# Kernel tuning notes

Hardware: AMD Instinct MI355X
Metric: run time of the kernel (lower is better)

## Reference

```python
import jax, jax.numpy as jnp
import numpy as np

K = 20          # neighbors
T = 3           # time steps
GW = 10.0       # surrogate-gradient width
EPS = 1e-5      # batchnorm eps


def _knn_idx(f, k):
    # f: (B, N, C). torch code maximizes -||xi-xj||^2 via topk.
    x2 = jnp.sum(f * f, axis=-1)                          # (B, N)
    inner = jnp.einsum('bnc,bmc->bnm', f, f)              # (B, N, N)
    neg_d = 2.0 * inner - x2[:, :, None] - x2[:, None, :]
    return jax.lax.top_k(neg_d, k)[1]                     # (B, N, k)


def _graph_feature(f, k):
    # f: (B, N, C) -> (B, N, k, 2C) = cat(neighbor - center, neighbor)
    idx = _knn_idx(f, k)
    nb = jax.vmap(lambda ft, ix: ft[ix])(f, idx)          # (B, N, k, C)
    return jnp.concatenate([nb - f[:, :, None, :], nb], axis=-1)


def _bn(x, g, b, axes):
    # training-mode batchnorm (batch statistics), channel-last
    m = jnp.mean(x, axis=axes, keepdims=True)
    v = jnp.var(x, axis=axes, keepdims=True)
    return (x - m) * jax.lax.rsqrt(v + EPS) * g + b


def _lrelu(x):
    return jnp.where(x >= 0, x, 0.2 * x)


def _spike(x):
    # surrogate value + straight-through hard spike (training-mode detach trick)
    xc = jnp.clip(x, -10.0, 10.0)
    soft = 0.5 * jnp.exp(-0.5 * xc * xc) / np.sqrt(2.0 * np.pi) + 0.5 * jax.nn.sigmoid(GW * xc)
    hard = (x > 0).astype(x.dtype)
    return soft + jax.lax.stop_gradient(hard - soft)


def _lif(x, mem, thr, ref, md, ta, rd, tb):
    md = jnp.clip(md, 0.1, 0.99)
    ta = jnp.clip(ta, 0.001, 0.1)
    rd = jnp.clip(rd, 0.1, 0.95)
    x = x * (ref <= 0).astype(x.dtype)
    mem = mem * md * (1.0 - ref) + x
    s = _spike(mem - thr)
    mem = mem * (1.0 - s)
    ref = ref * rd + s
    thr = tb + (thr + ta * s - tb) * 0.95
    return s, mem, thr, ref


def _forward(x, W0, g0, b0, W1, g1, b1, W2, g2, b2, W3, g3, b3, Wm, gm, bm,
             l0md, l0ta, l0rd, l0tb, l1md, l1ta, l1rd, l1tb,
             l2md, l2ta, l2rd, l2tb, l3md, l3ta, l3rd, l3tb,
             lfmd, lfta, lfrd, lftb, tw):
    f0 = jnp.transpose(x, (0, 2, 1))                      # (B, N, 3)
    convs = [(W0, g0, b0), (W1, g1, b1), (W2, g2, b2), (W3, g3, b3)]
    lifs = [(l0md, l0ta, l0rd, l0tb), (l1md, l1ta, l1rd, l1tb),
            (l2md, l2ta, l2rd, l2tb), (l3md, l3ta, l3rd, l3tb)]
    states = [None] * 4
    pooled = []
    for t in range(T):
        cur = f0
        feats = []
        for i in range(4):
            gf = _graph_feature(cur, K)                   # (B, N, k, 2C)
            h = jnp.einsum('bnkc,oc->bnko', gf, convs[i][0])  # 1x1 conv
            h = _lrelu(_bn(h, convs[i][1], convs[i][2], (0, 1, 2)))
            h = jnp.max(h, axis=2)                        # max over k -> (B, N, O)
            md, ta, rd, tb = lifs[i]
            if states[i] is None:
                mem = jnp.zeros_like(h)
                thr = jnp.broadcast_to(tb, h.shape).astype(h.dtype)
                ref = jnp.zeros_like(h)
            else:
                # state manager detaches persisted states between calls
                mem, thr, ref = (jax.lax.stop_gradient(s) for s in states[i])
            s, mem, thr, ref = _lif(h, mem, thr, ref, md, ta, rd, tb)
            states[i] = (mem, thr, ref)
            feats.append(s)
            cur = s
        cat = jnp.concatenate(feats, axis=-1)             # (B, N, 960)
        agg = _lrelu(_bn(jnp.einsum('bnc,oc->bno', cat, Wm), gm, bm, (0, 1)))
        pooled.append(jnp.max(agg, axis=1))               # global max pool -> (B, 512)
    tf = jnp.stack(pooled, axis=0)                        # (T, B, 512)
    out = jnp.einsum('t,tbf->bf', jax.nn.softmax(tw), tf)
    mem = jnp.zeros_like(out)
    thr = jnp.broadcast_to(lftb, out.shape).astype(out.dtype)
    ref = jnp.zeros_like(out)
    s, _, _, _ = _lif(out, mem, thr, ref, lfmd, lfta, lfrd, lftb)
    return s


def setup_inputs() -> dict:
    key = jax.random.key(0)
    ks = iter(jax.random.split(key, 64))
    B, N = 2, 1024
    d = {}
    d['x'] = jax.random.normal(next(ks), (B, 3, N), jnp.float32)
    dims = [(64, 6), (128, 128), (256, 256), (512, 512)]  # (out, in) for 1x1 convs
    for i, (o, c) in enumerate(dims):
        d[f'W{i}'] = jax.random.normal(next(ks), (o, c), jnp.float32) / np.sqrt(c)
        d[f'g{i}'] = 1.0 + 0.1 * jax.random.normal(next(ks), (o,), jnp.float32)
        d[f'b{i}'] = 0.1 * jax.random.normal(next(ks), (o,), jnp.float32)
    d['Wm'] = jax.random.normal(next(ks), (512, 960), jnp.float32) / np.sqrt(960.0)
    d['gm'] = 1.0 + 0.1 * jax.random.normal(next(ks), (512,), jnp.float32)
    d['bm'] = 0.1 * jax.random.normal(next(ks), (512,), jnp.float32)
    for name, c in [('l0', 64), ('l1', 128), ('l2', 256), ('l3', 512), ('lf', 512)]:
        d[name + 'md'] = jnp.full((c,), 0.9, jnp.float32) + 0.02 * jax.random.normal(next(ks), (c,), jnp.float32)
        d[name + 'ta'] = jnp.full((c,), 0.01, jnp.float32) + 0.002 * jax.random.normal(next(ks), (c,), jnp.float32)
        d[name + 'rd'] = jnp.full((c,), 0.5, jnp.float32) + 0.02 * jax.random.normal(next(ks), (c,), jnp.float32)
        d[name + 'tb'] = jnp.ones((c,), jnp.float32) + 0.05 * jax.random.normal(next(ks), (c,), jnp.float32)
    d['tw'] = 1.0 + 0.1 * jax.random.normal(next(ks), (T,), jnp.float32)
    return d


def reference(x, W0, g0, b0, W1, g1, b1, W2, g2, b2, W3, g3, b3, Wm, gm, bm,
              l0md, l0ta, l0rd, l0tb, l1md, l1ta, l1rd, l1tb,
              l2md, l2ta, l2rd, l2tb, l3md, l3ta, l3rd, l3tb,
              lfmd, lfta, lfrd, lftb, tw):
    return _forward(x, W0, g0, b0, W1, g1, b1, W2, g2, b2, W3, g3, b3, Wm, gm, bm,
                    l0md, l0ta, l0rd, l0tb, l1md, l1ta, l1rd, l1tb,
                    l2md, l2ta, l2rd, l2tb, l3md, l3ta, l3rd, l3tb,
                    lfmd, lfta, lfrd, lftb, tw)
```

## Files before the change

kernel.cpp:

```cpp
#include <hip/hip_runtime.h>
#include <math.h>

#define NPTS 1024
#define BB 2
#define KNN 20
#define ROWS 2048
#define CATC 960
#define TT 3
#define IDXS 32
typedef unsigned long long ull;
typedef __attribute__((ext_vector_type(8))) short bf16x8;
typedef __attribute__((ext_vector_type(4))) float f32x4;

__device__ __forceinline__ float lrelu_f(float x){ return x >= 0.f ? x : 0.2f*x; }
__device__ __forceinline__ unsigned short f2bf(float f){
  unsigned u = __float_as_uint(f);
  return (unsigned short)((u + 0x7FFFu + ((u >> 16) & 1u)) >> 16);
}
__device__ __forceinline__ float bf2f(unsigned short h){ return __uint_as_float(((unsigned)h) << 16); }

__device__ __forceinline__ void stg_u32(unsigned* p, unsigned v){ __hip_atomic_store(p, v, __ATOMIC_RELAXED, __HIP_MEMORY_SCOPE_AGENT); }
__device__ __forceinline__ void stg_f64(double* p, double v){ __hip_atomic_store(p, v, __ATOMIC_RELAXED, __HIP_MEMORY_SCOPE_AGENT); }
__device__ __forceinline__ unsigned ldg_u32(const unsigned* p){ return __hip_atomic_load(p, __ATOMIC_RELAXED, __HIP_MEMORY_SCOPE_AGENT); }
__device__ __forceinline__ double ldg_f64(const double* p){ return __hip_atomic_load(p, __ATOMIC_RELAXED, __HIP_MEMORY_SCOPE_AGENT); }

__device__ __forceinline__ void mfma_dev(const short* __restrict__ A, int lda,
    const short* __restrict__ B3, size_t sStride, int ldb,
    float* __restrict__ C, int ldc, int K, int bm, int bn, int tid)
{
  const int wave = tid >> 6, lane = tid & 63;
  const int wm = (wave >> 1) << 5, wn = (wave & 1) << 5;
  const int rr = lane & 15, kq = (lane >> 4) << 3;
  f32x4 acc[2][2] = {};
  const short* Ap = A + (size_t)(bm + wm + rr)*lda + kq;
  const short* Bp = B3 + (size_t)(bn + wn + rr)*ldb + kq;
  for (int k0 = 0; k0 < K; k0 += 32) {
    bf16x8 a0 = *(const bf16x8*)(Ap + k0);
    bf16x8 a1 = *(const bf16x8*)(Ap + (size_t)16*lda + k0);
#pragma unroll
    for (int s = 0; s < 3; ++s) {
      bf16x8 b0 = *(const bf16x8*)(Bp + (size_t)s*sStride + k0);
      bf16x8 b1 = *(const bf16x8*)(Bp + (size_t)s*sStride + (size_t)16*ldb + k0);
      acc[0][0] = __builtin_amdgcn_mfma_f32_16x16x32_bf16(a0, b0, acc[0][0], 0, 0, 0);
      acc[0][1] = __builtin_amdgcn_mfma_f32_16x16x32_bf16(a0, b1, acc[0][1], 0, 0, 0);
      acc[1][0] = __builtin_amdgcn_mfma_f32_16x16x32_bf16(a1, b0, acc[1][0], 0, 0, 0);
      acc[1][1] = __builtin_amdgcn_mfma_f32_16x16x32_bf16(a1, b1, acc[1][1], 0, 0, 0);
    }
  }
  const int drb = (lane >> 4) << 2;
#pragma unroll
  for (int i = 0; i < 2; ++i)
#pragma unroll
    for (int j = 0; j < 2; ++j)
#pragma unroll
      for (int t = 0; t < 4; ++t)
        C[(size_t)(bm + wm + i*16 + drb + t)*ldc + bn + wn + j*16 + rr] = acc[i][j][t];
}

__device__ __forceinline__ void agg_tile(const short* __restrict__ scat, const short* __restrict__ WmH,
    double* __restrict__ Sa1, double* __restrict__ Sa2, unsigned* __restrict__ mxe,
    int tm, int tn, int tid)
{
  const int wave = tid >> 6, lane = tid & 63;
  const int wm = (wave >> 1) << 5;
  const int wn = (wave & 1) << 4;
  const int rr = lane & 15, kq = (lane >> 4) << 3;
  const int bm = tm*64, bn = tn*32;
  f32x4 acc[2] = {};
  const short* Ap = scat + (size_t)(bm + wm + rr)*CATC + kq;
  const short* Bp = WmH + (size_t)(bn + wn + rr)*960 + kq;
  for (int k0 = 0; k0 < 960; k0 += 32){
    bf16x8 a0 = *(const bf16x8*)(Ap + k0);
    bf16x8 a1 = *(const bf16x8*)(Ap + (size_t)16*CATC + k0);
#pragma unroll
    for (int s = 0; s < 3; ++s){
      bf16x8 b0 = *(const bf16x8*)(Bp + (size_t)s*491520 + k0);
      acc[0] = __builtin_amdgcn_mfma_f32_16x16x32_bf16(a0, b0, acc[0], 0, 0, 0);
      acc[1] = __builtin_amdgcn_mfma_f32_16x16x32_bf16(a1, b0, acc[1], 0, 0, 0);
    }
  }
  double ds = 0.0, dq = 0.0; float mx = -INFINITY;
#pragma unroll
  for (int i = 0; i < 2; ++i)
#pragma unroll
    for (int t = 0; t < 4; ++t){
      float v = acc[i][t];
      ds += (double)v; dq += (double)v*(double)v; mx = fmaxf(mx, v);
    }
#pragma unroll
  for (int off = 16; off < 64; off <<= 1){
    ds += __shfl_xor(ds, off);
    dq += __shfl_xor(dq, off);
    float o = __shfl_xor(mx, off); mx = fmaxf(mx, o);
  }
  if (lane < 16){
    int col = bn + wn + lane;
    atomicAdd(&Sa1[col], ds);
    atomicAdd(&Sa2[col], dq);
    unsigned u = __float_as_uint(mx);
    u = (u & 0x80000000u) ? ~u : (u | 0x80000000u);
    atomicMax(&mxe[(bm >> 10)*512 + col], u);
  }
}

template<int W>
__device__ __forceinline__ void knn_wave(const ull* __restrict__ pk, int* __restrict__ idx,
                                         int row, int lane)
{
  const int n = row & (NPTS-1), b = row >> 10;
  const ull* pb = pk + (size_t)b*NPTS*W;
  ull cw[W]; int pn = 0;
#pragma unroll
  for (int w=0; w<W; ++w){ cw[w] = pb[(size_t)n*W + w]; pn += __popcll(cw[w]); }
  unsigned keys[16];
#pragma unroll 4
  for (int i=0;i<16;++i){
    int m = lane + (i<<6);
    int inner=0, pm=0;
#pragma unroll
    for (int w=0;w<W;++w){
      ull rm = pb[(size_t)m*W + w];
      inner += __popcll(rm & cw[w]);
      pm    += __popcll(rm);
    }
    int d = 2*inner - pn - pm;
    keys[i] = ((unsigned)(d+1024)<<11) | (unsigned)(NPTS-1-m);
  }
  unsigned lmax = keys[0];
#pragma unroll
  for (int i=1;i<16;++i) lmax = keys[i]>lmax ? keys[i] : lmax;
  unsigned mywin = 0;
  for (int s=0;s<KNN;++s){
    unsigned v = lmax;
#pragma unroll
    for (int off=1; off<64; off<<=1){ unsigned o = __shfl_xor(v, off, 64); if (o>v) v=o; }
    if (lane == s) mywin = (unsigned)(NPTS-1) - (v & 0x7FFu);
    if (lmax == v){
#pragma unroll
      for (int i=0;i<16;++i) if (keys[i]==v) keys[i]=0u;
      lmax = keys[0];
#pragma unroll
      for (int i=1;i<16;++i) lmax = keys[i]>lmax ? keys[i] : lmax;
    }
  }
  if (lane < KNN) idx[(size_t)row*IDXS + lane] = (int)mywin;
}

__device__ __forceinline__ void knn0_wave(const float* __restrict__ x, int* __restrict__ idx,
                                          int row, int lane)
{
  const int n = row & (NPTS-1), b = row >> 10;
  const float* xb = x + (size_t)b*3*NPTS;
  float fn0 = xb[n], fn1 = xb[NPTS+n], fn2 = xb[2*NPTS+n];
  float x2n = __fadd_rn(__fadd_rn(__fmul_rn(fn0,fn0), __fmul_rn(fn1,fn1)), __fmul_rn(fn2,fn2));
  ull keys[16];
#pragma unroll 4
  for (int i=0;i<16;++i){
    int m = lane + (i<<6);
    float a0 = xb[m], a1 = xb[NPTS+m], a2 = xb[2*NPTS+m];
    float x2m = __fadd_rn(__fadd_rn(__fmul_rn(a0,a0), __fmul_rn(a1,a1)), __fmul_rn(a2,a2));
    float inner = __fadd_rn(__fadd_rn(__fmul_rn(fn0,a0), __fmul_rn(fn1,a1)), __fmul_rn(fn2,a2));
    float v = __fsub_rn(__fsub_rn(__fmul_rn(2.f,inner), x2n), x2m);
    unsigned u = __float_as_uint(v);
    u = (u & 0x80000000u) ? ~u : (u | 0x80000000u);
    keys[i] = ((ull)u << 32) | (unsigned)(NPTS-1-m);
  }
  ull lmax = keys[0];
#pragma unroll
  for (int i=1;i<16;++i) lmax = keys[i]>lmax ? keys[i] : lmax;
  unsigned mywin = 0;
  for (int s=0;s<KNN;++s){
    ull v = lmax;
#pragma unroll
    for (int off=1; off<64; off<<=1){ ull o = __shfl_xor(v, off, 64); if (o>v) v=o; }
    if (lane == s) mywin = (unsigned)(NPTS-1) - (unsigned)(v & 0xFFFFFFFFull);
    if (lmax == v){
#pragma unroll
      for (int i=0;i<16;++i) if (keys[i]==v) keys[i]=0ull;
      lmax = keys[0];
#pragma unroll
      for (int i=1;i<16;++i) lmax = keys[i]>lmax ? keys[i] : lmax;
    }
  }
  if (lane < KNN) idx[(size_t)row*IDXS + lane] = (int)mywin;
}

__device__ __forceinline__ void conv0_dev(const float* __restrict__ x, const float* __restrict__ W0,
    float* __restrict__ AB0, int tile, int tid, float* sm)
{
  float (*As)[64] = (float(*)[64])sm;
  float (*Bs)[64] = (float(*)[64])(sm + 3*64);
  int bm = (tile >> 1) * 64, bn = (tile & 1) * 64;
  int b = bm >> 10, n0 = bm & (NPTS-1);
  if (tid < 192){ int k = tid >> 6, r = tid & 63; As[k][r] = x[(size_t)b*3072 + k*NPTS + n0 + r]; }
  if (tid >= 64){
    int k = (tid - 64) >> 6, c = (tid - 64) & 63; int row = bn + c;
    Bs[k][c] = (row < 64) ? __fadd_rn(W0[(size_t)row*6+k], W0[(size_t)row*6+3+k])
                          : W0[(size_t)(row-64)*6+k];
  }
  __syncthreads();
  const int tx = tid & 15, ty = tid >> 4;
  float acc[4][4] = {};
#pragma unroll
  for (int kk = 0; kk < 3; ++kk){
    float ar[4], br[4];
#pragma unroll
    for (int i=0;i<4;++i) ar[i] = As[kk][ty*4+i];
#pragma unroll
    for (int j=0;j<4;++j) br[j] = Bs[kk][tx*4+j];
#pragma unroll
    for (int i=0;i<4;++i)
#pragma unroll
      for (int j=0;j<4;++j) acc[i][j] = fmaf(ar[i], br[j], acc[i][j]);
  }
#pragma unroll
  for (int i=0;i<4;++i)
#pragma unroll
    for (int j=0;j<4;++j)
      AB0[(size_t)(bm+ty*4+i)*128 + bn+tx*4+j] = acc[i][j];
  __syncthreads();
}

__device__ __forceinline__ void wsplit_store(float w, short* dst, size_t NK, size_t e){
  unsigned short h1 = f2bf(w); float f1 = bf2f(h1);
  float r1 = w - f1;
  unsigned short h2 = f2bf(r1); float f2v = bf2f(h2);
  unsigned short h3 = f2bf(r1 - f2v);
  dst[e] = (short)h1; dst[NK + e] = (short)h2; dst[2*NK + e] = (short)h3;
}
__device__ __forceinline__ void wcatsplit(const float* __restrict__ W, short* __restrict__ dst,
                                          int O, int C, size_t e){
  int rr = (int)(e / C), cc = (int)(e - (size_t)rr*C);
  float w = (rr < O) ? __fadd_rn(W[(size_t)rr*2*C + cc], W[(size_t)rr*2*C + C + cc])
                     : W[(size_t)(rr-O)*2*C + cc];
  wsplit_store(w, dst, (size_t)2*O*C, e);
}

__device__ __forceinline__ float lif_step(float h, int o, size_t i, int init,
    double s1v, double s2v,
    const float* gv, const float* bv,
    const float* pmd, const float* pta, const float* prd, const float* ptb,
    float* sM, float* sT, float* sR)
{
  double cnt = (double)ROWS * (double)KNN;
  double mu = s1v / cnt;
  double vv = s2v / cnt - mu*mu;
  float mean = (float)mu;
  float inv  = 1.f / sqrtf((float)vv + 1e-5f);
  h = ((h - mean) * inv) * gv[o] + bv[o];
  h = lrelu_f(h);
  float md = fminf(fmaxf(pmd[o], 0.1f), 0.99f);
  float ta = fminf(fmaxf(pta[o], 0.001f), 0.1f);
  float rd = fminf(fmaxf(prd[o], 0.1f), 0.95f);
  float tb = ptb[o];
  float M, T, R;
  if (init) { M = 0.f; T = tb; R = 0.f; }
  else      { M = sM[i]; T = sT[i]; R = sR[i]; }
  float xv = (R <= 0.f) ? h : 0.f;
  M = M * md * (1.f - R) + xv;
  float sp = (M - T > 0.f) ? 1.f : 0.f;
  M = M * (1.f - sp);
  R = R * rd + sp;
  T = tb + (T + ta*sp - tb) * 0.95f;
  sM[i] = M; sT[i] = T; sR[i] = R;
  return sp;
}
__device__ __forceinline__ void emit_spike(float sp, short* scat, size_t row, int off, int o,
                                           ull* pk, size_t i, int tid)
{
  scat[row*CATC + off + o] = (sp != 0.f) ? (short)0x3F80 : (short)0;
  ull ball = __ballot(sp != 0.f);
  if ((tid & 63) == 0) pk[i >> 6] = ball;
}

__global__ __launch_bounds__(256) void k_setup(
    const float* W1, const float* W2, const float* W3, const float* Wm,
    short* wcH1, short* wcH2, short* wcH3, short* WmH,
    double* S12all, double* aggD, unsigned* aggM, unsigned* cnt)
{
  int vb = blockIdx.x, tid = threadIdx.x;
  if (vb < 10){ for (int j=tid; j<1024; j+=256) stg_f64(S12all + (size_t)vb*1024 + j, 0.0); }
  else if (vb < 13){ int t = vb-10;
    for (int j=tid; j<1024; j+=256){ stg_f64(aggD + (size_t)t*1024 + j, 0.0); stg_u32(aggM + (size_t)t*1024 + j, 0u); } }
  else if (vb < 14){ if (tid < 16) stg_u32(cnt + tid, 0u); }
  else if (vb < 78)   wcatsplit(W1, wcH1, 128,  64, (size_t)(vb-14)*256 + tid);
  else if (vb < 334)  wcatsplit(W2, wcH2, 256, 128, (size_t)(vb-78)*256 + tid);
  else if (vb < 1358) wcatsplit(W3, wcH3, 512, 256, (size_t)(vb-334)*256 + tid);
  else                wsplit_store(Wm[(size_t)(vb-1358)*256 + tid], WmH, (size_t)512*960, (size_t)(vb-1358)*256 + tid);
}

__global__ __launch_bounds__(256) void k_nt0(const float* __restrict__ x, const float* __restrict__ W0,
                                             int* __restrict__ idx0, float* __restrict__ AB0)
{
  __shared__ __align__(16) float sm[6*64];
  int bid = blockIdx.x, tid = threadIdx.x;
  if (bid < 512) knn0_wave(x, idx0, bid*4 + (tid>>6), tid & 63);
  else           conv0_dev(x, W0, AB0, bid - 512, tid, sm);
}

__global__ __launch_bounds__(256) void k_gather2(const float* __restrict__ AB, const int* __restrict__ idx,
    float* __restrict__ hmaxS, double* __restrict__ S12, int O, int OC, int RPB)
{
  __shared__ double red[2][4][64];
  const int bid = blockIdx.x, tid = threadIdx.x;
  const int wave = tid >> 6, lane = tid & 63;
  const int oc = bid % OC, rc = bid / OC;
  const int o = oc*64 + lane;
  const int twoO = 2*O;
  const int rstart = rc * RPB;
  double ts1 = 0.0, ts2 = 0.0;
  for (int r = rstart + wave; r < rstart + RPB; r += 4){
    int b = r >> 10;
    const float* ABb = AB + (size_t)(b*NPTS)*twoO + o;
    float bc = AB[(size_t)r*twoO + O + o];
    const int* ip = idx + (size_t)r*IDXS;
    float mx = -INFINITY; double s1 = 0.0, s2 = 0.0;
#pragma unroll
    for (int k = 0; k < KNN; ++k){
      int m = ip[k];
      float a = ABb[(size_t)m*twoO];
      mx = fmaxf(mx, a); s1 += (double)a; s2 += (double)a*(double)a;
    }
    hmaxS[(size_t)r*O + o] = mx - bc;
    ts1 += s1 - (double)KNN*(double)bc;
    ts2 += s2 - 2.0*(double)bc*s1 + (double)KNN*(double)bc*(double)bc;
  }
  red[0][wave][lane] = ts1;
  red[1][wave][lane] = ts2;
  __syncthreads();
  if (wave == 0){
    double a = red[0][0][lane] + red[0][1][lane] + red[0][2][lane] + red[0][3][lane];
    double q = red[1][0][lane] + red[1][1][lane] + red[1][2][lane] + red[1][3][lane];
    atomicAdd(&S12[o], a);
    atomicAdd(&S12[512 + o], q);
  }
}

__global__ __launch_bounds__(256) void k_lif0agg(const float* __restrict__ hmax0, const double* __restrict__ S12_0,
    const float* gv, const float* bv, const float* pmd, const float* pta, const float* prd, const float* ptb,
    float* sM, float* sT, float* sR, short* __restrict__ scat, ull* __restrict__ pk0, int init,
    const short* __restrict__ scatPrev, const short* __restrict__ WmH,
    double* __restrict__ aggDt, unsigned* __restrict__ aggMt)
{
  int bid = blockIdx.x, tid = threadIdx.x;
  if (bid < 512){
    int i = bid*256 + tid, o = i & 63;
    size_t row = (size_t)(i >> 6);
    float sp = lif_step(hmax0[i], o, (size_t)i, init, S12_0[o], S12_0[512+o],
                        gv, bv, pmd, pta, prd, ptb, sM, sT, sR);
    emit_spike(sp, scat, row, 0, o, pk0, (size_t)i, tid);
  } else {
    int tile = bid - 512;
    agg_tile(scatPrev, WmH, aggDt, aggDt + 512, aggMt, tile >> 4, tile & 15, tid);
  }
}

template<int W>
__global__ __launch_bounds__(256) void k_knnconv(const ull* __restrict__ pk, int* __restrict__ idx,
    const short* __restrict__ Ain, const short* __restrict__ wcH,
    float* __restrict__ AB, int twoO, int K, int ntn)
{
  int bid = blockIdx.x, tid = threadIdx.x;
  if (bid < 512) knn_wave<W>(pk, idx, bid*4 + (tid>>6), tid & 63);
  else {
    int id = bid - 512, tm = id/ntn, tn = id - tm*ntn;
    mfma_dev(Ain, CATC, wcH, (size_t)twoO*K, K, AB, twoO, K, tm*64, tn*64, tid);
  }
}

__global__ __launch_bounds__(256) void k_bnlif(const float* __restrict__ hmaxS, int oShift,
    const double* __restrict__ S12,
    const float* gv, const float* bv, const float* pmd, const float* pta, const float* prd, const float* ptb,
    float* sM, float* sT, float* sR, short* __restrict__ scat, int offOut,
    ull* __restrict__ pkOut, int init)
{
  int i = blockIdx.x*256 + threadIdx.x;
  int O = 1 << oShift;
  int o = i & (O-1);
  size_t row = (size_t)(i >> oShift);
  float sp = lif_step(hmaxS[i], o, (size_t)i, init, S12[o], S12[512+o],
                      gv, bv, pmd, pta, prd, ptb, sM, sT, sR);
  emit_spike(sp, scat, row, offOut, o, pkOut, (size_t)i, threadIdx.x);
}

__global__ __launch_bounds__(256) void k_aggfin(const short* __restrict__ scat2, const short* __restrict__ WmH,
    double* __restrict__ aggD, unsigned* __restrict__ aggM, unsigned* __restrict__ cnt,
    const float* gm, const float* bmv, const float* tw, const float* lftb, float* __restrict__ out)
{
  int bid = blockIdx.x, tid = threadIdx.x;
  if (bid < 512){
    agg_tile(scat2, WmH, aggD + 2048, aggD + 2048 + 512, aggM + 2048, bid >> 4, bid & 15, tid);
    asm volatile("s_waitcnt vmcnt(0)" ::: "memory");
    __syncthreads();
    if (tid == 0) __hip_atomic_fetch_add(cnt, 1u, __ATOMIC_RELAXED, __HIP_MEMORY_SCOPE_AGENT);
  } else {
    if (tid == 0) while (ldg_u32(cnt) < 512u) __builtin_amdgcn_s_sleep(4);
    __syncthreads();
    int i = (bid - 512)*256 + tid;
    int b = i >> 9, o = i & 511;
    float pool[3];
#pragma unroll
    for (int t = 0; t < 3; ++t){
      double s1v = ldg_f64(&aggD[(size_t)t*1024 + o]);
      double s2v = ldg_f64(&aggD[(size_t)t*1024 + 512 + o]);
      double mean = s1v / (double)ROWS;
      float var = (float)(s2v / (double)ROWS - mean*mean);
      float m = (float)mean;
      float inv = 1.f / sqrtf(var + 1e-5f);
      unsigned e = ldg_u32(&aggM[(size_t)t*1024 + b*512 + o]);
      unsigned u = (e & 0x80000000u) ? (e & 0x7FFFFFFFu) : ~e;
      float mx = __uint_as_float(u);
      pool[t] = lrelu_f(((mx - m)*inv)*gm[o] + bmv[o]);
    }
    float t0 = tw[0], t1 = tw[1], t2 = tw[2];
    float mxw = fmaxf(t0, fmaxf(t1, t2));
    float e0 = expf(t0-mxw), e1 = expf(t1-mxw), e2 = expf(t2-mxw);
    float den = e0 + e1 + e2;
    float v = (e0/den)*pool[0] + (e1/den)*pool[1] + (e2/den)*pool[2];
    out[i] = (v - lftb[o] > 0.f) ? 1.f : 0.f;
  }
}

extern "C" void kernel_launch(void* const* d_in, const int* in_sizes, int n_in,
                              void* d_out, int out_size, void* d_ws, size_t ws_size,
                              hipStream_t stream)
{
  (void)in_sizes; (void)n_in; (void)out_size; (void)ws_size;
  const float* x = (const float*)d_in[0];
  const float* Wl[4] = {(const float*)d_in[1],(const float*)d_in[4],(const float*)d_in[7],(const float*)d_in[10]};
  const float* gl[4] = {(const float*)d_in[2],(const float*)d_in[5],(const float*)d_in[8],(const float*)d_in[11]};
  const float* bl[4] = {(const float*)d_in[3],(const float*)d_in[6],(const float*)d_in[9],(const float*)d_in[12]};
  const float* Wm = (const float*)d_in[13];
  const float* gm = (const float*)d_in[14];
  const float* bm = (const float*)d_in[15];
  const float* lp[5][4];
  for (int l = 0; l < 5; ++l)
    for (int q = 0; q < 4; ++q)
      lp[l][q] = (const float*)d_in[16 + l*4 + q];
  const float* tw = (const float*)d_in[36];

  char* pw = (char*)d_ws;
  auto alloc = [&](size_t bytes)->char* {
    char* r = pw; pw += (bytes + 255) & ~(size_t)255; return r;
  };
  int*    idx0  = (int*)   alloc((size_t)ROWS*IDXS*sizeof(int));
  int*    idxS  = (int*)   alloc((size_t)ROWS*IDXS*sizeof(int));
  float*  AB0   = (float*) alloc((size_t)ROWS*128*sizeof(float));
  float*  AB    = (float*) alloc((size_t)ROWS*1024*sizeof(float));
  float*  hmax0 = (float*) alloc((size_t)ROWS*64*sizeof(float));
  float*  hmaxS = (float*) alloc((size_t)ROWS*512*sizeof(float));
  double* S12   = (double*)alloc((size_t)10*1024*sizeof(double));
  short*  scatH[3];
  for (int t = 0; t < 3; ++t) scatH[t] = (short*)alloc((size_t)ROWS*CATC*sizeof(short));
  int Wn[4] = {1, 2, 4, 8};
  ull* pk[4];
  for (int l = 0; l < 4; ++l) pk[l] = (ull*)alloc((size_t)ROWS*Wn[l]*sizeof(ull));
  double*   aggD = (double*)  alloc((size_t)3*1024*sizeof(double));
  unsigned* aggM = (unsigned*)alloc((size_t)3*1024*sizeof(unsigned));
  short* wcH[4];
  wcH[1] = (short*)alloc((size_t)3*2*128*64*sizeof(short));
  wcH[2] = (short*)alloc((size_t)3*2*256*128*sizeof(short));
  wcH[3] = (short*)alloc((size_t)3*2*512*256*sizeof(short));
  short* WmH = (short*)alloc((size_t)3*512*960*sizeof(short));
  int Oo[4] = {64, 128, 256, 512};
  float *stM[4], *stT[4], *stR[4];
  for (int l = 0; l < 4; ++l){
    stM[l] = (float*)alloc((size_t)ROWS*Oo[l]*sizeof(float));
    stT[l] = (float*)alloc((size_t)ROWS*Oo[l]*sizeof(float));
    stR[l] = (float*)alloc((size_t)ROWS*Oo[l]*sizeof(float));
  }
  unsigned* cnt = (unsigned*)alloc(256);

  k_setup<<<3278, 256, 0, stream>>>(Wl[1], Wl[2], Wl[3], Wm,
                                    wcH[1], wcH[2], wcH[3], WmH, S12, aggD, aggM, cnt);
  k_nt0<<<576, 256, 0, stream>>>(x, Wl[0], idx0, AB0);
  k_gather2<<<512, 256, 0, stream>>>(AB0, idx0, hmax0, S12, 64, 1, 4);

  int Cin[4]  = {3, 64, 128, 256};
  int offIn[4]= {0, 0, 64, 192};
  int offOut[4]={0, 64, 192, 448};

  for (int t = 0; t < TT; ++t){
    int init = (t == 0) ? 1 : 0;
    int grid0 = init ? 512 : 1024;
    k_lif0agg<<<grid0, 256, 0, stream>>>(hmax0, S12, gl[0], bl[0],
        lp[0][0], lp[0][1], lp[0][2], lp[0][3],
        stM[0], stT[0], stR[0], scatH[t], pk[0], init,
        init ? (const short*)nullptr : scatH[t-1], WmH,
        aggD + (size_t)(init ? 0 : (t-1))*1024, aggM + (size_t)(init ? 0 : (t-1))*1024);
    for (int li = 1; li < 4; ++li){
      int C = Cin[li], O = Oo[li], twoO = 2*O, ntn = twoO/64, nConv = 32*ntn;
      const short* fin = scatH[t] + offIn[li];
      double* S12i = S12 + (size_t)(1 + t*3 + (li-1))*1024;
      switch (Wn[li-1]){
        case 1: k_knnconv<1><<<512+nConv, 256, 0, stream>>>(pk[0], idxS, fin, wcH[li], AB, twoO, C, ntn); break;
        case 2: k_knnconv<2><<<512+nConv, 256, 0, stream>>>(pk[1], idxS, fin, wcH[li], AB, twoO, C, ntn); break;
        default: k_knnconv<4><<<512+nConv, 256, 0, stream>>>(pk[2], idxS, fin, wcH[li], AB, twoO, C, ntn); break;
      }
      int OC = O/64;
      k_gather2<<<512, 256, 0, stream>>>(AB, idxS, hmaxS, S12i, O, OC, 4*OC);
      int oSh = (O==128)?7:(O==256)?8:9;
      k_bnlif<<<(ROWS*O)/256, 256, 0, stream>>>(hmaxS, oSh, S12i,
          gl[li], bl[li], lp[li][0], lp[li][1], lp[li][2], lp[li][3],
          stM[li], stT[li], stR[li], scatH[t], offOut[li], pk[li], init);
    }
  }
  k_aggfin<<<516, 256, 0, stream>>>(scatH[2], WmH, aggD, aggM, cnt + 9,
                                    gm, bm, tw, lp[4][3], (float*)d_out);
}
```

Measured before the change: 481.7 us.

## Fold layer-0 LIF into bnlif tail and agg tiles into knnconv launch

Drops the separate per-step lif0agg launch. The layer-0 LIF for the next time step now runs as extra tail blocks of the last bnlif launch of the current step, and the previous step's aggregation GEMM tiles run as extra blocks of the first knnconv launch. The aggregation tile grows from 64x32 to 64x64, so half as many blocks each reuse their A loads across two B column tiles. This cuts kernel launches and overlaps independent work, at the cost of more registers per agg block and a more complex grid layout.

```diff
diff --git a/kernel.cpp b/kernel.cpp
--- a/kernel.cpp
+++ b/kernel.cpp
@@ -57,16 +57,16 @@
         C[(size_t)(bm + wm + i*16 + drb + t)*ldc + bn + wn + j*16 + rr] = acc[i][j][t];
 }
 
-__device__ __forceinline__ void agg_tile(const short* __restrict__ scat, const short* __restrict__ WmH,
+__device__ __forceinline__ void agg_tile64(const short* __restrict__ scat, const short* __restrict__ WmH,
     double* __restrict__ Sa1, double* __restrict__ Sa2, unsigned* __restrict__ mxe,
     int tm, int tn, int tid)
 {
   const int wave = tid >> 6, lane = tid & 63;
   const int wm = (wave >> 1) << 5;
-  const int wn = (wave & 1) << 4;
+  const int wn = (wave & 1) << 5;
   const int rr = lane & 15, kq = (lane >> 4) << 3;
-  const int bm = tm*64, bn = tn*32;
-  f32x4 acc[2] = {};
+  const int bm = tm*64, bn = tn*64;
+  f32x4 acc[2][2] = {};
   const short* Ap = scat + (size_t)(bm + wm + rr)*CATC + kq;
   const short* Bp = WmH + (size_t)(bn + wn + rr)*960 + kq;
   for (int k0 = 0; k0 < 960; k0 += 32){
@@ -75,31 +75,37 @@
 #pragma unroll
     for (int s = 0; s < 3; ++s){
       bf16x8 b0 = *(const bf16x8*)(Bp + (size_t)s*491520 + k0);
-      acc[0] = __builtin_amdgcn_mfma_f32_16x16x32_bf16(a0, b0, acc[0], 0, 0, 0);
-      acc[1] = __builtin_amdgcn_mfma_f32_16x16x32_bf16(a1, b0, acc[1], 0, 0, 0);
-    }
-  }
-  double ds = 0.0, dq = 0.0; float mx = -INFINITY;
-#pragma unroll
-  for (int i = 0; i < 2; ++i)
-#pragma unroll
-    for (int t = 0; t < 4; ++t){
-      float v = acc[i][t];
-      ds += (double)v; dq += (double)v*(double)v; mx = fmaxf(mx, v);
-    }
-#pragma unroll
-  for (int off = 16; off < 64; off <<= 1){
-    ds += __shfl_xor(ds, off);
-    dq += __shfl_xor(dq, off);
-    float o = __shfl_xor(mx, off); mx = fmaxf(mx, o);
-  }
-  if (lane < 16){
-    int col = bn + wn + lane;
-    atomicAdd(&Sa1[col], ds);
-    atomicAdd(&Sa2[col], dq);
-    unsigned u = __float_as_uint(mx);
-    u = (u & 0x80000000u) ? ~u : (u | 0x80000000u);
-    atomicMax(&mxe[(bm >> 10)*512 + col], u);
+      bf16x8 b1 = *(const bf16x8*)(Bp + (size_t)s*491520 + (size_t)16*960 + k0);
+      acc[0][0] = __builtin_amdgcn_mfma_f32_16x16x32_bf16(a0, b0, acc[0][0], 0, 0, 0);
+      acc[0][1] = __builtin_amdgcn_mfma_f32_16x16x32_bf16(a0, b1, acc[0][1], 0, 0, 0);
+      acc[1][0] = __builtin_amdgcn_mfma_f32_16x16x32_bf16(a1, b0, acc[1][0], 0, 0, 0);
+      acc[1][1] = __builtin_amdgcn_mfma_f32_16x16x32_bf16(a1, b1, acc[1][1], 0, 0, 0);
+    }
+  }
+#pragma unroll
+  for (int j = 0; j < 2; ++j){
+    double ds = 0.0, dq = 0.0; float mx = -INFINITY;
+#pragma unroll
+    for (int i = 0; i < 2; ++i)
+#pragma unroll
+      for (int t = 0; t < 4; ++t){
+        float v = acc[i][j][t];
+        ds += (double)v; dq += (double)v*(double)v; mx = fmaxf(mx, v);
+      }
+#pragma unroll
+    for (int off = 16; off < 64; off <<= 1){
+      ds += __shfl_xor(ds, off);
+      dq += __shfl_xor(dq, off);
+      float o = __shfl_xor(mx, off); mx = fmaxf(mx, o);
+    }
+    if (lane < 16){
+      int col = bn + wn + j*16 + lane;
+      atomicAdd(&Sa1[col], ds);
+      atomicAdd(&Sa2[col], dq);
+      unsigned u = __float_as_uint(mx);
+      u = (u & 0x80000000u) ? ~u : (u | 0x80000000u);
+      atomicMax(&mxe[(bm >> 10)*512 + col], u);
+    }
   }
 }
 
@@ -336,35 +342,32 @@
   }
 }
 
-__global__ __launch_bounds__(256) void k_lif0agg(const float* __restrict__ hmax0, const double* __restrict__ S12_0,
+__global__ __launch_bounds__(256) void k_lif0(const float* __restrict__ hmax0, const double* __restrict__ S12_0,
     const float* gv, const float* bv, const float* pmd, const float* pta, const float* prd, const float* ptb,
-    float* sM, float* sT, float* sR, short* __restrict__ scat, ull* __restrict__ pk0, int init,
-    const short* __restrict__ scatPrev, const short* __restrict__ WmH,
-    double* __restrict__ aggDt, unsigned* __restrict__ aggMt)
-{
-  int bid = blockIdx.x, tid = threadIdx.x;
-  if (bid < 512){
-    int i = bid*256 + tid, o = i & 63;
-    size_t row = (size_t)(i >> 6);
-    float sp = lif_step(hmax0[i], o, (size_t)i, init, S12_0[o], S12_0[512+o],
-                        gv, bv, pmd, pta, prd, ptb, sM, sT, sR);
-    emit_spike(sp, scat, row, 0, o, pk0, (size_t)i, tid);
-  } else {
-    int tile = bid - 512;
-    agg_tile(scatPrev, WmH, aggDt, aggDt + 512, aggMt, tile >> 4, tile & 15, tid);
-  }
+    float* sM, float* sT, float* sR, short* __restrict__ scat, ull* __restrict__ pk0)
+{
+  int i = blockIdx.x*256 + threadIdx.x, o = i & 63;
+  size_t row = (size_t)(i >> 6);
+  float sp = lif_step(hmax0[i], o, (size_t)i, 1, S12_0[o], S12_0[512+o],
+                      gv, bv, pmd, pta, prd, ptb, sM, sT, sR);
+  emit_spike(sp, scat, row, 0, o, pk0, (size_t)i, threadIdx.x);
 }
 
 template<int W>
 __global__ __launch_bounds__(256) void k_knnconv(const ull* __restrict__ pk, int* __restrict__ idx,
     const short* __restrict__ Ain, const short* __restrict__ wcH,
-    float* __restrict__ AB, int twoO, int K, int ntn)
+    float* __restrict__ AB, int twoO, int K, int ntn,
+    const short* __restrict__ scatPrev, const short* __restrict__ WmH,
+    double* __restrict__ aggDt, unsigned* __restrict__ aggMt, int nMain)
 {
   int bid = blockIdx.x, tid = threadIdx.x;
   if (bid < 512) knn_wave<W>(pk, idx, bid*4 + (tid>>6), tid & 63);
-  else {
+  else if (bid < nMain){
     int id = bid - 512, tm = id/ntn, tn = id - tm*ntn;
     mfma_dev(Ain, CATC, wcH, (size_t)twoO*K, K, AB, twoO, K, tm*64, tn*64, tid);
+  } else {
+    int tile = bid - nMain;
+    agg_tile64(scatPrev, WmH, aggDt, aggDt + 512, aggMt, tile >> 3, tile & 7, tid);
   }
 }
 
@@ -372,15 +375,27 @@
     const double* __restrict__ S12,
     const float* gv, const float* bv, const float* pmd, const float* pta, const float* prd, const float* ptb,
     float* sM, float* sT, float* sR, short* __restrict__ scat, int offOut,
-    ull* __restrict__ pkOut, int init)
-{
-  int i = blockIdx.x*256 + threadIdx.x;
-  int O = 1 << oShift;
-  int o = i & (O-1);
-  size_t row = (size_t)(i >> oShift);
-  float sp = lif_step(hmaxS[i], o, (size_t)i, init, S12[o], S12[512+o],
-                      gv, bv, pmd, pta, prd, ptb, sM, sT, sR);
-  emit_spike(sp, scat, row, offOut, o, pkOut, (size_t)i, threadIdx.x);
+    ull* __restrict__ pkOut, int init, int nMain,
+    const float* __restrict__ hmax0, const double* __restrict__ S12_0,
+    const float* g0, const float* b0, const float* pmd0, const float* pta0, const float* prd0, const float* ptb0,
+    float* sM0, float* sT0, float* sR0, short* __restrict__ scatN, ull* __restrict__ pk0)
+{
+  int bid = blockIdx.x, tid = threadIdx.x;
+  if (bid < nMain){
+    int i = bid*256 + tid;
+    int O = 1 << oShift;
+    int o = i & (O-1);
+    size_t row = (size_t)(i >> oShift);
+    float sp = lif_step(hmaxS[i], o, (size_t)i, init, S12[o], S12[512+o],
+                        gv, bv, pmd, pta, prd, ptb, sM, sT, sR);
+    emit_spike(sp, scat, row, offOut, o, pkOut, (size_t)i, tid);
+  } else {
+    int i = (bid - nMain)*256 + tid, o = i & 63;
+    size_t row = (size_t)(i >> 6);
+    float sp = lif_step(hmax0[i], o, (size_t)i, 0, S12_0[o], S12_0[512+o],
+                        g0, b0, pmd0, pta0, prd0, ptb0, sM0, sT0, sR0);
+    emit_spike(sp, scatN, row, 0, o, pk0, (size_t)i, tid);
+  }
 }
 
 __global__ __launch_bounds__(256) void k_aggfin(const short* __restrict__ scat2, const short* __restrict__ WmH,
@@ -388,15 +403,15 @@
     const float* gm, const float* bmv, const float* tw, const float* lftb, float* __restrict__ out)
 {
   int bid = blockIdx.x, tid = threadIdx.x;
-  if (bid < 512){
-    agg_tile(scat2, WmH, aggD + 2048, aggD + 2048 + 512, aggM + 2048, bid >> 4, bid & 15, tid);
+  if (bid < 256){
+    agg_tile64(scat2, WmH, aggD + 2048, aggD + 2048 + 512, aggM + 2048, bid >> 3, bid & 7, tid);
     asm volatile("s_waitcnt vmcnt(0)" ::: "memory");
     __syncthreads();
     if (tid == 0) __hip_atomic_fetch_add(cnt, 1u, __ATOMIC_RELAXED, __HIP_MEMORY_SCOPE_AGENT);
   } else {
-    if (tid == 0) while (ldg_u32(cnt) < 512u) __builtin_amdgcn_s_sleep(4);
+    if (tid == 0) while (ldg_u32(cnt) < 256u) __builtin_amdgcn_s_sleep(4);
     __syncthreads();
-    int i = (bid - 512)*256 + tid;
+    int i = (bid - 256)*256 + tid;
     int b = i >> 9, o = i & 511;
     float pool[3];
 #pragma unroll
@@ -475,6 +490,9 @@
                                     wcH[1], wcH[2], wcH[3], WmH, S12, aggD, aggM, cnt);
   k_nt0<<<576, 256, 0, stream>>>(x, Wl[0], idx0, AB0);
   k_gather2<<<512, 256, 0, stream>>>(AB0, idx0, hmax0, S12, 64, 1, 4);
+  k_lif0<<<512, 256, 0, stream>>>(hmax0, S12, gl[0], bl[0],
+      lp[0][0], lp[0][1], lp[0][2], lp[0][3],
+      stM[0], stT[0], stR[0], scatH[0], pk[0]);
 
   int Cin[4]  = {3, 64, 128, 256};
   int offIn[4]= {0, 0, 64, 192};
@@ -482,29 +500,36 @@
 
   for (int t = 0; t < TT; ++t){
     int init = (t == 0) ? 1 : 0;
-    int grid0 = init ? 512 : 1024;
-    k_lif0agg<<<grid0, 256, 0, stream>>>(hmax0, S12, gl[0], bl[0],
-        lp[0][0], lp[0][1], lp[0][2], lp[0][3],
-        stM[0], stT[0], stR[0], scatH[t], pk[0], init,
-        init ? (const short*)nullptr : scatH[t-1], WmH,
-        aggD + (size_t)(init ? 0 : (t-1))*1024, aggM + (size_t)(init ? 0 : (t-1))*1024);
     for (int li = 1; li < 4; ++li){
       int C = Cin[li], O = Oo[li], twoO = 2*O, ntn = twoO/64, nConv = 32*ntn;
       const short* fin = scatH[t] + offIn[li];
       double* S12i = S12 + (size_t)(1 + t*3 + (li-1))*1024;
+      int nMain2 = 512 + nConv;
+      int hasAgg = (li == 1 && t > 0) ? 1 : 0;
+      int gridK = nMain2 + (hasAgg ? 256 : 0);
+      const short* scPrev = hasAgg ? scatH[t-1] : (const short*)nullptr;
+      double* aggDt = aggD + (size_t)(hasAgg ? (t-1) : 0)*1024;
+      unsigned* aggMt = aggM + (size_t)(hasAgg ? (t-1) : 0)*1024;
       switch (Wn[li-1]){
-        case 1: k_knnconv<1><<<512+nConv, 256, 0, stream>>>(pk[0], idxS, fin, wcH[li], AB, twoO, C, ntn); break;
-        case 2: k_knnconv<2><<<512+nConv, 256, 0, stream>>>(pk[1], idxS, fin, wcH[li], AB, twoO, C, ntn); break;
-        default: k_knnconv<4><<<512+nConv, 256, 0, stream>>>(pk[2], idxS, fin, wcH[li], AB, twoO, C, ntn); break;
+        case 1: k_knnconv<1><<<gridK, 256, 0, stream>>>(pk[0], idxS, fin, wcH[li], AB, twoO, C, ntn,
+                    scPrev, WmH, aggDt, aggMt, nMain2); break;
+        case 2: k_knnconv<2><<<gridK, 256, 0, stream>>>(pk[1], idxS, fin, wcH[li], AB, twoO, C, ntn,
+                    scPrev, WmH, aggDt, aggMt, nMain2); break;
+        default: k_knnconv<4><<<gridK, 256, 0, stream>>>(pk[2], idxS, fin, wcH[li], AB, twoO, C, ntn,
+                    scPrev, WmH, aggDt, aggMt, nMain2); break;
       }
       int OC = O/64;
       k_gather2<<<512, 256, 0, stream>>>(AB, idxS, hmaxS, S12i, O, OC, 4*OC);
       int oSh = (O==128)?7:(O==256)?8:9;
-      k_bnlif<<<(ROWS*O)/256, 256, 0, stream>>>(hmaxS, oSh, S12i,
+      int nMainB = (ROWS*O)/256;
+      int tailLif0 = (li == 3 && t < 2) ? 512 : 0;
+      k_bnlif<<<nMainB + tailLif0, 256, 0, stream>>>(hmaxS, oSh, S12i,
           gl[li], bl[li], lp[li][0], lp[li][1], lp[li][2], lp[li][3],
-          stM[li], stT[li], stR[li], scatH[t], offOut[li], pk[li], init);
-    }
-  }
-  k_aggfin<<<516, 256, 0, stream>>>(scatH[2], WmH, aggD, aggM, cnt + 9,
+          stM[li], stT[li], stR[li], scatH[t], offOut[li], pk[li], init, nMainB,
+          hmax0, S12, gl[0], bl[0], lp[0][0], lp[0][1], lp[0][2], lp[0][3],
+          stM[0], stT[0], stR[0], (t < 2) ? scatH[t+1] : (short*)nullptr, pk[0]);
+    }
+  }
+  k_aggfin<<<260, 256, 0, stream>>>(scatH[2], WmH, aggD, aggM, cnt + 9,
                                     gm, bm, tw, lp[4][3], (float*)d_out);
 }
```

Result: faster. 435.0 us (-9.7%).
